# Kernel tuning notes

Hardware: AMD Instinct MI355X
Metric: run time of the kernel (lower is better)

## Reference

```python
import jax, jax.numpy as jnp
import numpy as np

N_CLASSES = 100
EPSILON = 1e-07


def setup_inputs() -> dict:
    key = jax.random.key(0)
    k1, k2 = jax.random.split(key)
    y_pred = jax.random.normal(k1, (1_000_000, N_CLASSES), dtype=jnp.float32)
    y_true = jax.random.randint(k2, (1_000_000,), 0, N_CLASSES, dtype=jnp.int64 if jax.config.jax_enable_x64 else jnp.int32)
    return {"y_pred": y_pred, "y_true": y_true}


def _confusion_matrix(y_pred, y_true, n_classes):
    # vectorized scatter-add 2D histogram: cm[t, p] += 1
    p = jnp.argmax(y_pred, axis=1)
    t = y_true.reshape(-1).astype(jnp.int32)
    p = p.reshape(-1).astype(jnp.int32)
    cm = jnp.zeros((n_classes, n_classes), dtype=jnp.float32)
    return cm.at[t, p].add(1.0)


def reference(y_pred, y_true):
    C = N_CLASSES
    cm = _confusion_matrix(y_pred, y_true, C)  # [C, C]
    total = cm.sum()
    row_sum = cm.sum(axis=1)   # actual-class marginals
    col_sum = cm.sum(axis=0)   # predicted-class marginals
    diag = jnp.diagonal(cm)
    # For label l: TN = total - row_sum[l] - col_sum[l] + cm[l,l]; FP = col? No:
    # FP = conf_matrix[l, idx].sum() = row_sum[l] - diag[l]
    TN = total - row_sum - col_sum + diag
    FP = row_sum - diag
    specificity = jnp.sum(TN / (TN + FP + EPSILON)) / C
    return specificity
```

## Files before the change

### kernel.cpp

```cpp
#include <hip/hip_runtime.h>
#include <math.h>

#define N_CLASSES 100
#define EPSILON 1e-7f


__global__ void zero_counters(int* __restrict__ cnt) {
    int i = threadIdx.x;
    if (i < 3 * N_CLASSES) cnt[i] = 0;
}

__global__ __launch_bounds__(256)
void argmax_hist(const float* __restrict__ y_pred,
                 const int* __restrict__ y_true,
                 int* __restrict__ cnt, int n_rows) {
    __shared__ int h_true[N_CLASSES];
    __shared__ int h_pred[N_CLASSES];
    __shared__ int h_diag[N_CLASSES];
    for (int i = threadIdx.x; i < N_CLASSES; i += blockDim.x) {
        h_true[i] = 0; h_pred[i] = 0; h_diag[i] = 0;
    }
    __syncthreads();

    int row    = blockIdx.x * blockDim.x + threadIdx.x;
    int stride = gridDim.x * blockDim.x;
    for (; row < n_rows; row += stride) {
        const float4* p = reinterpret_cast<const float4*>(
            y_pred + (size_t)row * N_CLASSES);
        float best = -INFINITY;
        int   bi   = 0;
        #pragma unroll
        for (int j = 0; j < 25; ++j) {
            float4 v = p[j];
            int base = j * 4;
            if (v.x > best) { best = v.x; bi = base;     }
            if (v.y > best) { best = v.y; bi = base + 1; }
            if (v.z > best) { best = v.z; bi = base + 2; }
            if (v.w > best) { best = v.w; bi = base + 3; }
        }
        int t = y_true[row];
        atomicAdd(&h_true[t], 1);
        atomicAdd(&h_pred[bi], 1);
        if (t == bi) atomicAdd(&h_diag[t], 1);
    }

    __syncthreads();
    for (int i = threadIdx.x; i < N_CLASSES; i += blockDim.x) {
        int a = h_true[i], b = h_pred[i], c = h_diag[i];
        if (a) atomicAdd(&cnt[i], a);
        if (b) atomicAdd(&cnt[N_CLASSES + i], b);
        if (c) atomicAdd(&cnt[2 * N_CLASSES + i], c);
    }
}

__global__ void finalize(const int* __restrict__ cnt,
                         float* __restrict__ out, int n_rows) {
    __shared__ float partial[128];
    int i = threadIdx.x;
    float v = 0.0f;
    if (i < N_CLASSES) {
        float row_sum = (float)cnt[i];
        float col_sum = (float)cnt[N_CLASSES + i];
        float diag    = (float)cnt[2 * N_CLASSES + i];
        float total   = (float)n_rows;
        float TN = total - row_sum - col_sum + diag;
        float FP = row_sum - diag;
        v = TN / (TN + FP + EPSILON);
    }
    partial[i] = v;
    __syncthreads();
    for (int s = 64; s > 0; s >>= 1) {
        if (i < s) partial[i] += partial[i + s];
        __syncthreads();
    }
    if (i == 0) out[0] = partial[0] / (float)N_CLASSES;
}

extern "C" void kernel_launch(void* const* d_in, const int* in_sizes, int n_in,
                              void* d_out, int out_size, void* d_ws, size_t ws_size,
                              hipStream_t stream) {
    const float* y_pred = (const float*)d_in[0];
    const int*   y_true = (const int*)d_in[1];
    int n_rows = in_sizes[1];

    int*   cnt = (int*)d_ws;
    float* out = (float*)d_out;

    zero_counters<<<1, 384, 0, stream>>>(cnt);

    int blocks = (n_rows + 255) / 256;
    argmax_hist<<<blocks, 256, 0, stream>>>(y_pred, y_true, cnt, n_rows);

    finalize<<<1, 128, 0, stream>>>(cnt, out, n_rows);
}
```

Measured before the change: 629.0 us.

## Split each row's argmax across 16 lanes with shuffle-based key reduction

Instead of one thread scanning a whole 400-byte row, each group of 16 lanes loads consecutive float4 chunks of the same row, so global loads are coalesced. Per-lane maxima are packed into a monotone 64-bit key (value, inverted index) and reduced with xor shuffles, which keeps the first-index tie-break. The grid is fixed at 2048 blocks with a grid-stride loop. In exchange, only lane 0 updates the histogram, and lanes 9-15 sit idle on the second chunk.

```diff
diff --git a/kernel.cpp b/kernel.cpp
--- a/kernel.cpp
+++ b/kernel.cpp
@@ -22,26 +22,47 @@
     }
     __syncthreads();
 
-    int row    = blockIdx.x * blockDim.x + threadIdx.x;
-    int stride = gridDim.x * blockDim.x;
-    for (; row < n_rows; row += stride) {
-        const float4* p = reinterpret_cast<const float4*>(
+    const int sub = threadIdx.x & 15;
+    const int q   = (blockIdx.x * blockDim.x + threadIdx.x) >> 4;
+    const int Q   = (gridDim.x * blockDim.x) >> 4;
+
+    for (int row = q; row < n_rows; row += Q) {
+        const float4* rp4 = reinterpret_cast<const float4*>(
             y_pred + (size_t)row * N_CLASSES);
-        float best = -INFINITY;
-        int   bi   = 0;
+
+        float4 v0 = rp4[sub];
+        float best = v0.x; int bi = 4 * sub;
+        if (v0.y > best) { best = v0.y; bi = 4 * sub + 1; }
+        if (v0.z > best) { best = v0.z; bi = 4 * sub + 2; }
+        if (v0.w > best) { best = v0.w; bi = 4 * sub + 3; }
+
+        if (sub < 9) {
+            float4 v1 = rp4[16 + sub];
+            int b2 = 64 + 4 * sub;
+            if (v1.x > best) { best = v1.x; bi = b2;     }
+            if (v1.y > best) { best = v1.y; bi = b2 + 1; }
+            if (v1.z > best) { best = v1.z; bi = b2 + 2; }
+            if (v1.w > best) { best = v1.w; bi = b2 + 3; }
+        }
+
+        unsigned u = __float_as_uint(best);
+        unsigned mono = u ^ (unsigned)(((int)u >> 31) | 0x80000000);
+        unsigned long long key =
+            ((unsigned long long)mono << 32) | (unsigned)(~bi);
+
         #pragma unroll
-        for (int j = 0; j < 25; ++j) {
-            float4 v = p[j];
-            int base = j * 4;
-            if (v.x > best) { best = v.x; bi = base;     }
-            if (v.y > best) { best = v.y; bi = base + 1; }
-            if (v.z > best) { best = v.z; bi = base + 2; }
-            if (v.w > best) { best = v.w; bi = base + 3; }
+        for (int m = 1; m <= 8; m <<= 1) {
+            unsigned long long other = __shfl_xor(key, m, 16);
+            if (other > key) key = other;
         }
-        int t = y_true[row];
-        atomicAdd(&h_true[t], 1);
-        atomicAdd(&h_pred[bi], 1);
-        if (t == bi) atomicAdd(&h_diag[t], 1);
+
+        if (sub == 0) {
+            int rbi = (int)(~(unsigned)(key & 0xffffffffull));
+            int t = y_true[row];
+            atomicAdd(&h_true[t], 1);
+            atomicAdd(&h_pred[rbi], 1);
+            if (t == rbi) atomicAdd(&h_diag[t], 1);
+        }
     }
 
     __syncthreads();
@@ -88,8 +109,7 @@
 
     zero_counters<<<1, 384, 0, stream>>>(cnt);
 
-    int blocks = (n_rows + 255) / 256;
-    argmax_hist<<<blocks, 256, 0, stream>>>(y_pred, y_true, cnt, n_rows);
+    argmax_hist<<<2048, 256, 0, stream>>>(y_pred, y_true, cnt, n_rows);
 
     finalize<<<1, 128, 0, stream>>>(cnt, out, n_rows);
 }
```

Result: faster. 557.4 us (-11.4%).
